# Kernel optimization log

Measured on AMD Instinct MI355X. Metric: run time of the kernel, lower is better.

## Reference

```python
import jax, jax.numpy as jnp
import numpy as np

N0 = 65536   # input features (e.g. 256x256 photoreceptors)
N1 = 16384   # layer-0 nodes
K0 = 32      # fan-in of layer-0 nodes
N2 = 150     # layer-1 nodes (must be 150 to feed fc1: Linear(150, 2))
K1 = 64      # fan-in of layer-1 nodes
B = 64       # batch


def setup_inputs() -> dict:
    key = jax.random.key(0)
    ks = jax.random.split(key, 9)
    return {
        "x":     jax.random.normal(ks[0], (B, N0), dtype=jnp.float32),
        "conn0": jax.random.randint(ks[1], (N1, K0), 0, N0, dtype=jnp.int32),
        "conn1": jax.random.randint(ks[2], (N2, K1), 0, N1, dtype=jnp.int32),
        "W0":    jax.random.normal(ks[3], (N1, K0), dtype=jnp.float32) * (1.0 / np.sqrt(K0)),
        "b0":    jax.random.normal(ks[4], (N1,), dtype=jnp.float32) * 0.01,
        "W1":    jax.random.normal(ks[5], (N2, K1), dtype=jnp.float32) * (1.0 / np.sqrt(K1)),
        "b1":    jax.random.normal(ks[6], (N2,), dtype=jnp.float32) * 0.01,
        "fc_w":  jax.random.normal(ks[7], (2, N2), dtype=jnp.float32) * (1.0 / np.sqrt(N2)),
        "fc_b":  jax.random.normal(ks[8], (2,), dtype=jnp.float32) * 0.01,
    }


def _sparse_layer(prev, conn, W, b):
    # prev: [B, Nprev], conn: [n, k] indices into Nprev, W: [n, k], b: [n]
    gathered = prev[:, conn]                      # [B, n, k] irregular gather
    return jax.nn.relu(jnp.einsum('bnk,nk->bn', gathered, W) + b)


def reference(x, conn0, conn1, W0, b0, W1, b1, fc_w, fc_b):
    h = _sparse_layer(x, conn0, W0, b0)           # [B, N1]
    h = _sparse_layer(h, conn1, W1, b1)           # [B, N2]
    return h @ fc_w.T + fc_b                      # [B, 2]
```

## Files before the change

### kernel.cpp

```cpp
#include <hip/hip_runtime.h>
#include <hip/hip_bf16.h>

#define N0 65536
#define N1 16384
#define K0 32
#define N2 150
#define K1 64
#define BB 64


__global__ __launch_bounds__(256) void k_transpose(const float* __restrict__ x,
                                                   const int* __restrict__ conn1,
                                                   __hip_bfloat16* __restrict__ xT,
                                                   unsigned char* __restrict__ used) {
    __shared__ float tile[64][65];
    const int c0 = blockIdx.x << 6;
    const int t  = threadIdx.x;
    const int rr = t >> 4;
    const int c4 = (t & 15) << 2;
#pragma unroll
    for (int i = 0; i < 4; ++i) {
        const int row = (i << 4) + rr;
        const float4 v = *(const float4*)(x + (size_t)row * N0 + c0 + c4);
        tile[row][c4 + 0] = v.x;
        tile[row][c4 + 1] = v.y;
        tile[row][c4 + 2] = v.z;
        tile[row][c4 + 3] = v.w;
    }
    __syncthreads();
    const int cc = t & 63;
    const int r4 = t >> 6;
#pragma unroll
    for (int i = 0; i < 16; ++i) {
        const int c = (r4 << 4) + i;
        xT[(size_t)(c0 + c) * BB + cc] = __float2bfloat16(tile[cc][c]);
    }
    const int g = (blockIdx.x << 8) + t;
    if (g < N2 * K1) used[conn1[g]] = 1;
}

__global__ __launch_bounds__(256, 8) void k_layer0(const __hip_bfloat16* __restrict__ xT,
                                                   const int*   __restrict__ conn0,
                                                   const float* __restrict__ W0,
                                                   const float* __restrict__ b0,
                                                   const unsigned char* __restrict__ used,
                                                   const float* __restrict__ fc_b,
                                                   float* __restrict__ out,
                                                   __hip_bfloat16* __restrict__ h0T) {
    if (blockIdx.x == 0 && threadIdx.x < BB * 2) {
        out[threadIdx.x] = fc_b[threadIdx.x & 1];
    }
    const int lane = threadIdx.x & 63;
    const int n = __builtin_amdgcn_readfirstlane((blockIdx.x << 2) + (threadIdx.x >> 6));
    if (used[n] != 1) return;
    const int*   __restrict__ cp = conn0 + (n << 5);
    const float* __restrict__ wp = W0 + (n << 5);
    float acc = 0.f;
#pragma unroll 16
    for (int k = 0; k < K0; ++k) {
        acc = fmaf(__bfloat162float(xT[((size_t)cp[k] << 6) + lane]), wp[k], acc);
    }
    acc += b0[n];
    h0T[(n << 6) + lane] = __float2bfloat16(fmaxf(acc, 0.f));
}

__global__ __launch_bounds__(256) void k_layer1fc(const __hip_bfloat16* __restrict__ h0T,
                                                  const int*   __restrict__ conn1,
                                                  const float* __restrict__ W1,
                                                  const float* __restrict__ b1,
                                                  const float* __restrict__ fc_w,
                                                  float* __restrict__ out) {
    const int lane = threadIdx.x & 63;
    const int n = __builtin_amdgcn_readfirstlane((blockIdx.x << 2) + (threadIdx.x >> 6));
    if (n >= N2) return;
    const int*   __restrict__ cp = conn1 + (n << 6);
    const float* __restrict__ wp = W1 + (n << 6);
    float acc = 0.f;
#pragma unroll 32
    for (int k = 0; k < K1; ++k) {
        acc = fmaf(__bfloat162float(h0T[((size_t)cp[k] << 6) + lane]), wp[k], acc);
    }
    const float h1 = fmaxf(acc + b1[n], 0.f);
    const float w0 = fc_w[n];
    const float w1 = fc_w[N2 + n];
    atomicAdd(&out[(lane << 1) + 0], h1 * w0);
    atomicAdd(&out[(lane << 1) + 1], h1 * w1);
}

extern "C" void kernel_launch(void* const* d_in, const int* in_sizes, int n_in,
                              void* d_out, int out_size, void* d_ws, size_t ws_size,
                              hipStream_t stream) {
    const float* x     = (const float*)d_in[0];
    const int*   conn0 = (const int*)  d_in[1];
    const int*   conn1 = (const int*)  d_in[2];
    const float* W0    = (const float*)d_in[3];
    const float* b0    = (const float*)d_in[4];
    const float* W1    = (const float*)d_in[5];
    const float* b1    = (const float*)d_in[6];
    const float* fc_w  = (const float*)d_in[7];
    const float* fc_b  = (const float*)d_in[8];
    float* out = (float*)d_out;

    char* ws = (char*)d_ws;
    __hip_bfloat16* xT  = (__hip_bfloat16*)(ws);
    __hip_bfloat16* h0T = (__hip_bfloat16*)(ws + (size_t)N0 * BB * 2);
    unsigned char* used = (unsigned char*)(ws + (size_t)N0 * BB * 2
                                              + (size_t)N1 * BB * 2);

    k_transpose<<<N0 / 64, 256, 0, stream>>>(x, conn1, xT, used);
    k_layer0<<<N1 / 4, 256, 0, stream>>>(xT, conn0, W0, b0, used, fc_b, out, h0T);
    k_layer1fc<<<(N2 + 3) / 4, 256, 0, stream>>>(h0T, conn1, W1, b1, fc_w, out);
}
```

Baseline: 99.46 us.

## Pack bf16 pairs in transpose stores and split layer-1 fan-in across warps

The transpose kernel now writes two bf16 values per 32-bit store instead of single 16-bit stores, which halves the number of store instructions for the dominant write of xT. The layer-1 kernel uses one block per node with four wavefronts, each covering a quarter of the fan-in, and reduces the partial sums through shared memory. This raises parallelism from 38 blocks to 150. The output bias initialisation moves from layer0 into the transpose kernel. The cost is an extra shared-memory reduction and a block barrier in layer1.

```diff
diff --git a/kernel.cpp b/kernel.cpp
--- a/kernel.cpp
+++ b/kernel.cpp
@@ -9,13 +9,22 @@
 #define BB 64
 
 
+__device__ __forceinline__ unsigned int pack_bf16(float lo, float hi) {
+    unsigned int l = __bfloat16_as_ushort(__float2bfloat16(lo));
+    unsigned int h = __bfloat16_as_ushort(__float2bfloat16(hi));
+    return (h << 16) | l;
+}
+
 __global__ __launch_bounds__(256) void k_transpose(const float* __restrict__ x,
                                                    const int* __restrict__ conn1,
+                                                   const float* __restrict__ fc_b,
+                                                   float* __restrict__ out,
                                                    __hip_bfloat16* __restrict__ xT,
                                                    unsigned char* __restrict__ used) {
     __shared__ float tile[64][65];
     const int c0 = blockIdx.x << 6;
     const int t  = threadIdx.x;
+    if (blockIdx.x == 0 && t < BB * 2) out[t] = fc_b[t & 1];
     const int rr = t >> 4;
     const int c4 = (t & 15) << 2;
 #pragma unroll
@@ -28,12 +37,15 @@
         tile[row][c4 + 3] = v.w;
     }
     __syncthreads();
-    const int cc = t & 63;
-    const int r4 = t >> 6;
+    unsigned int* __restrict__ xT2 = (unsigned int*)xT;
+    const int bp   = t & 31;
+    const int half = (t >> 5) & 1;
+    const int cq   = t >> 6;
 #pragma unroll
-    for (int i = 0; i < 16; ++i) {
-        const int c = (r4 << 4) + i;
-        xT[(size_t)(c0 + c) * BB + cc] = __float2bfloat16(tile[cc][c]);
+    for (int i = 0; i < 8; ++i) {
+        const int c = (cq << 4) + (i << 1) + half;
+        xT2[((size_t)(c0 + c) << 5) + bp] =
+            pack_bf16(tile[(bp << 1) + 0][c], tile[(bp << 1) + 1][c]);
     }
     const int g = (blockIdx.x << 8) + t;
     if (g < N2 * K1) used[conn1[g]] = 1;
@@ -44,12 +56,7 @@
                                                    const float* __restrict__ W0,
                                                    const float* __restrict__ b0,
                                                    const unsigned char* __restrict__ used,
-                                                   const float* __restrict__ fc_b,
-                                                   float* __restrict__ out,
                                                    __hip_bfloat16* __restrict__ h0T) {
-    if (blockIdx.x == 0 && threadIdx.x < BB * 2) {
-        out[threadIdx.x] = fc_b[threadIdx.x & 1];
-    }
     const int lane = threadIdx.x & 63;
     const int n = __builtin_amdgcn_readfirstlane((blockIdx.x << 2) + (threadIdx.x >> 6));
     if (used[n] != 1) return;
@@ -70,21 +77,25 @@
                                                   const float* __restrict__ b1,
                                                   const float* __restrict__ fc_w,
                                                   float* __restrict__ out) {
+    __shared__ float part[4][64];
     const int lane = threadIdx.x & 63;
-    const int n = __builtin_amdgcn_readfirstlane((blockIdx.x << 2) + (threadIdx.x >> 6));
-    if (n >= N2) return;
-    const int*   __restrict__ cp = conn1 + (n << 6);
-    const float* __restrict__ wp = W1 + (n << 6);
+    const int w    = threadIdx.x >> 6;
+    const int n    = blockIdx.x;
+    const int*   __restrict__ cp = conn1 + (n << 6) + (w << 4);
+    const float* __restrict__ wp = W1   + (n << 6) + (w << 4);
     float acc = 0.f;
-#pragma unroll 32
-    for (int k = 0; k < K1; ++k) {
+#pragma unroll
+    for (int k = 0; k < 16; ++k) {
         acc = fmaf(__bfloat162float(h0T[((size_t)cp[k] << 6) + lane]), wp[k], acc);
     }
-    const float h1 = fmaxf(acc + b1[n], 0.f);
-    const float w0 = fc_w[n];
-    const float w1 = fc_w[N2 + n];
-    atomicAdd(&out[(lane << 1) + 0], h1 * w0);
-    atomicAdd(&out[(lane << 1) + 1], h1 * w1);
+    part[w][lane] = acc;
+    __syncthreads();
+    if (w == 0) {
+        const float s = part[0][lane] + part[1][lane] + part[2][lane] + part[3][lane];
+        const float h1 = fmaxf(s + b1[n], 0.f);
+        atomicAdd(&out[(lane << 1) + 0], h1 * fc_w[n]);
+        atomicAdd(&out[(lane << 1) + 1], h1 * fc_w[N2 + n]);
+    }
 }
 
 extern "C" void kernel_launch(void* const* d_in, const int* in_sizes, int n_in,
@@ -107,7 +118,7 @@
     unsigned char* used = (unsigned char*)(ws + (size_t)N0 * BB * 2
                                               + (size_t)N1 * BB * 2);
 
-    k_transpose<<<N0 / 64, 256, 0, stream>>>(x, conn1, xT, used);
-    k_layer0<<<N1 / 4, 256, 0, stream>>>(xT, conn0, W0, b0, used, fc_b, out, h0T);
-    k_layer1fc<<<(N2 + 3) / 4, 256, 0, stream>>>(h0T, conn1, W1, b1, fc_w, out);
+    k_transpose<<<N0 / 64, 256, 0, stream>>>(x, conn1, fc_b, out, xT, used);
+    k_layer0<<<N1 / 4, 256, 0, stream>>>(xT, conn0, W0, b0, used, h0T);
+    k_layer1fc<<<N2, 256, 0, stream>>>(h0T, conn1, W1, b1, fc_w, out);
 }
```

New measurement: 97.73 us. Within noise of the previous version (-1.7%).
